# Kernel optimization log

Measured on AMD Instinct MI355X. Metric: run time of the kernel, lower is better.

The kernel has to match this reference:

```python
import jax, jax.numpy as jnp
import numpy as np

EMB = 1024
HEADS = 16
HEAD_DIM = EMB // HEADS
EPS = 1e-5


def setup_inputs() -> dict:
    key = jax.random.key(0)
    ks = jax.random.split(key, 10)
    B, T, D = 2, 2048, EMB
    s = 1.0 / np.sqrt(D)
    inp = {
        "x": jax.random.normal(ks[0], (B, T, D), dtype=jnp.float32),
        "wq": jax.random.normal(ks[1], (D, D), dtype=jnp.float32) * s,
        "bq": jnp.zeros((D,), jnp.float32),
        "wk": jax.random.normal(ks[2], (D, D), dtype=jnp.float32) * s,
        "bk": jnp.zeros((D,), jnp.float32),
        "wv": jax.random.normal(ks[3], (D, D), dtype=jnp.float32) * s,
        "bv": jnp.zeros((D,), jnp.float32),
        "wo": jax.random.normal(ks[4], (D, D), dtype=jnp.float32) * s,
        "bo": jnp.zeros((D,), jnp.float32),
        "gamma": jnp.ones((D,), jnp.float32),
        "beta": jnp.zeros((D,), jnp.float32),
    }
    return inp


def _attention(x, wq, bq, wk, bk, wv, bv, wo, bo, gamma, beta):
    B, T, D = x.shape
    H, Hd = HEADS, HEAD_DIM
    q = (x @ wq + bq).reshape(B, T, H, Hd)
    k = (x @ wk + bk).reshape(B, T, H, Hd)
    v = (x @ wv + bv).reshape(B, T, H, Hd)
    # scores: [B, H, T, T]
    scores = jnp.einsum("bthd,bshd->bhts", q, k) / np.sqrt(Hd)
    attn = jax.nn.softmax(scores, axis=-1)  # dropout is identity in eval
    ctx = jnp.einsum("bhts,bshd->bthd", attn, v).reshape(B, T, D)
    out = ctx @ wo + bo
    y = x + out  # residual (dropout identity)
    mu = jnp.mean(y, axis=-1, keepdims=True)
    var = jnp.var(y, axis=-1, keepdims=True)
    return (y - mu) * jax.lax.rsqrt(var + EPS) * gamma + beta


def reference(x, wq, bq, wk, bk, wv, bv, wo, bo, gamma, beta):
    return _attention(x, wq, bq, wk, bk, wv, bv, wo, bo, gamma, beta)
```

## Files before the change

### kernel.cpp

```cpp
#include <hip/hip_runtime.h>

#define BSZ   2
#define TSEQ  2048
#define DMOD  1024
#define NHEAD 16
#define HDIM  64
#define MROW  (BSZ*TSEQ)
#define LNEPS 1e-5f
#define QSCALE 0.18033688011f

typedef __bf16 bf16x8 __attribute__((ext_vector_type(8)));
typedef float  f32x4  __attribute__((ext_vector_type(4)));
typedef unsigned short us8 __attribute__((ext_vector_type(8)));
typedef unsigned short us4 __attribute__((ext_vector_type(4)));

__device__ __forceinline__ unsigned short f2bf(float f) {
    unsigned u = __float_as_uint(f);
    u += 0x7FFF + ((u >> 16) & 1);
    return (unsigned short)(u >> 16);
}
__device__ __forceinline__ float bf2f(unsigned short u) {
    return __uint_as_float((unsigned)u << 16);
}

__device__ __forceinline__ float fexp2(float x) {
#if __has_builtin(__builtin_amdgcn_exp2f)
    return __builtin_amdgcn_exp2f(x);
#else
    return __expf(x * 0.6931471805599453f);
#endif
}

__device__ __forceinline__ void gld_lds16(const void* g, void* l) {
    __builtin_amdgcn_global_load_lds(
        (const __attribute__((address_space(1))) unsigned int*)g,
        (__attribute__((address_space(3))) unsigned int*)l, 16, 0, 0);
}

__global__ __launch_bounds__(256) void prep_k(
    const float* __restrict__ x,
    const float* __restrict__ wq, const float* __restrict__ wk,
    const float* __restrict__ wv, const float* __restrict__ wo,
    unsigned short* __restrict__ Xb,
    unsigned short* __restrict__ WqkvT, unsigned short* __restrict__ WoT)
{
    const int tid = threadIdx.x;
    if (blockIdx.x < 2048) {
        const size_t i = ((size_t)blockIdx.x * 256 + tid) * 8;
        float4 a = *(const float4*)&x[i];
        float4 b = *(const float4*)&x[i + 4];
        union { unsigned short u[8]; uint4 v; } o;
        o.u[0]=f2bf(a.x); o.u[1]=f2bf(a.y); o.u[2]=f2bf(a.z); o.u[3]=f2bf(a.w);
        o.u[4]=f2bf(b.x); o.u[5]=f2bf(b.y); o.u[6]=f2bf(b.z); o.u[7]=f2bf(b.w);
        *(uint4*)&Xb[i] = o.v;
        return;
    }
    __shared__ float T[64][68];
    const int id = blockIdx.x - 2048;
    const int z  = id >> 8;
    const int bx = id & 15;
    const int by = (id >> 4) & 15;
    const float* W = (z == 0) ? wq : (z == 1) ? wk : (z == 2) ? wv : wo;
    unsigned short* Wt = (z < 3) ? (WqkvT + (size_t)z*1024*1024) : WoT;
    const int lr = tid >> 4, lc = (tid & 15) * 4;
    #pragma unroll
    for (int p = 0; p < 4; ++p) {
        const int kk = p*16 + lr;
        float4 v = *(const float4*)&W[(size_t)(by*64 + kk)*1024 + bx*64 + lc];
        T[lc+0][kk] = v.x; T[lc+1][kk] = v.y; T[lc+2][kk] = v.z; T[lc+3][kk] = v.w;
    }
    __syncthreads();
    #pragma unroll
    for (int p = 0; p < 2; ++p) {
        const int nl = p*32 + (tid >> 3);
        const int kb = (tid & 7) * 8;
        float4 a = *(const float4*)&T[nl][kb];
        float4 b = *(const float4*)&T[nl][kb+4];
        union { unsigned short u[8]; uint4 v; } o;
        o.u[0]=f2bf(a.x); o.u[1]=f2bf(a.y); o.u[2]=f2bf(a.z); o.u[3]=f2bf(a.w);
        o.u[4]=f2bf(b.x); o.u[5]=f2bf(b.y); o.u[6]=f2bf(b.z); o.u[7]=f2bf(b.w);
        *(uint4*)&Wt[(size_t)(bx*64 + nl)*1024 + by*64 + kb] = o.v;
    }
}


#define PH_SYNC() do { __builtin_amdgcn_s_barrier(); \
    asm volatile("s_waitcnt lgkmcnt(0)" ::: "memory"); \
    __builtin_amdgcn_sched_barrier(0); } while (0)

struct Core8 {
    const unsigned short *sA, *sB;
    unsigned short *A0w, *A1w, *B0w, *B1w;
    const unsigned short *fA0, *fA1, *fB0, *fB1;
    int swz0, swz1;
};

__device__ __forceinline__ void stage2(const unsigned short* s, unsigned short* d) {
    gld_lds16(s, d);
    gld_lds16(s + 64*1024, d + 4096);
}

__device__ __forceinline__ void core_setup(Core8& C, unsigned short* LDS,
    const unsigned short* A, const unsigned short* Bt, int bm, int bn, int kbase)
{
    const int tid = threadIdx.x;
    const int w = tid >> 6, lane = tid & 63;
    const int quad = lane >> 4, l16 = lane & 15;
    const int wm = w >> 2, wn = w & 3;
    const int r_l = lane >> 3, c_l = lane & 7;
    C.sA = A  + (size_t)(bm + w*8 + r_l)*1024 + (c_l ^ r_l)*8 + kbase;
    C.sB = Bt + (size_t)(bn + w*8 + r_l)*1024 + (c_l ^ r_l)*8 + kbase;
    unsigned short* A0 = LDS;
    unsigned short* A1 = LDS + 16384;
    unsigned short* B0 = LDS + 32768;
    unsigned short* B1 = LDS + 49152;
    C.A0w = A0 + w*512; C.A1w = A1 + w*512;
    C.B0w = B0 + w*512; C.B1w = B1 + w*512;
    C.fA0 = A0 + (wm*128 + l16)*64; C.fA1 = A1 + (wm*128 + l16)*64;
    C.fB0 = B0 + (wn*64 + l16)*64;  C.fB1 = B1 + (wn*64 + l16)*64;
    C.swz0 = ( quad      ^ (l16 & 7)) * 8;
    C.swz1 = ((4 + quad) ^ (l16 & 7)) * 8;
}

__device__ __forceinline__ void ld_b(const Core8& C, bf16x8 (&bfr)[4][2],
                                     const unsigned short* fB) {
    #pragma unroll
    for (int n = 0; n < 4; ++n) {
        bfr[n][0] = *(const bf16x8*)(fB + n*1024 + C.swz0);
        bfr[n][1] = *(const bf16x8*)(fB + n*1024 + C.swz1);
    }
}

template<int Q>
__device__ __forceinline__ void ld_a(const Core8& C, bf16x8 (&af)[2][2],
                                     const unsigned short* fA) {
    #pragma unroll
    for (int dm = 0; dm < 2; ++dm) {
        af[dm][0] = *(const bf16x8*)(fA + (Q*2+dm)*1024 + C.swz0);
        af[dm][1] = *(const bf16x8*)(fA + (Q*2+dm)*1024 + C.swz1);
    }
}

template<int Q>
__device__ __forceinline__ void mma_q(f32x4 (&acc)[8][4], bf16x8 (&af)[2][2],
                                      bf16x8 (&bfr)[4][2]) {
    __builtin_amdgcn_s_setprio(1);
    #pragma unroll
    for (int dm = 0; dm < 2; ++dm)
        #pragma unroll
        for (int n = 0; n < 4; ++n) {
            f32x4 t = acc[Q*2+dm][n];
            t = __builtin_amdgcn_mfma_f32_16x16x32_bf16(af[dm][0], bfr[n][0], t, 0, 0, 0);
            t = __builtin_amdgcn_mfma_f32_16x16x32_bf16(af[dm][1], bfr[n][1], t, 0, 0, 0);
            acc[Q*2+dm][n] = t;
        }
    __builtin_amdgcn_s_setprio(0);
}

template<int NIT>
__device__ __forceinline__ void core_kloop(const Core8& C, f32x4 (&acc)[8][4])
{
    stage2(C.sA,                 C.A0w);
    stage2(C.sA + 128*1024,      C.A0w + 8192);
    stage2(C.sB,                 C.B0w);
    stage2(C.sB + 128*1024,      C.B0w + 8192);
    stage2(C.sB + 64,            C.B1w);
    stage2(C.sB + 128*1024 + 64, C.B1w + 8192);
    asm volatile("s_waitcnt vmcnt(4)" ::: "memory");
    __builtin_amdgcn_s_barrier();

    bf16x8 bfr[4][2];
    bf16x8 af[2][2];

    #pragma unroll 1
    for (int it = 0; it < NIT - 1; ++it) {
        const int kk = it * 128;
        ld_b(C, bfr, C.fB0);
        ld_a<0>(C, af, C.fA0);
        stage2(C.sA + kk + 64,            C.A1w);
        stage2(C.sA + 128*1024 + kk + 64, C.A1w + 8192);
        PH_SYNC();  mma_q<0>(acc, af, bfr);
        __builtin_amdgcn_s_barrier();
        ld_a<1>(C, af, C.fA0);
        stage2(C.sB + kk + 128, C.B0w);
        PH_SYNC();  mma_q<1>(acc, af, bfr);
        __builtin_amdgcn_s_barrier();
        ld_a<2>(C, af, C.fA0);
        stage2(C.sB + 128*1024 + kk + 128, C.B0w + 8192);
        PH_SYNC();  mma_q<2>(acc, af, bfr);
        __builtin_amdgcn_s_barrier();
        ld_a<3>(C, af, C.fA0);
        PH_SYNC();  mma_q<3>(acc, af, bfr);
        asm volatile("s_waitcnt vmcnt(4)" ::: "memory");
        __builtin_amdgcn_s_barrier();
        ld_b(C, bfr, C.fB1);
        ld_a<0>(C, af, C.fA1);
        stage2(C.sA + kk + 128,            C.A0w);
        stage2(C.sA + 128*1024 + kk + 128, C.A0w + 8192);
        PH_SYNC();  mma_q<0>(acc, af, bfr);
        __builtin_amdgcn_s_barrier();
        ld_a<1>(C, af, C.fA1);
        stage2(C.sB + kk + 192, C.B1w);
        PH_SYNC();  mma_q<1>(acc, af, bfr);
        __builtin_amdgcn_s_barrier();
        ld_a<2>(C, af, C.fA1);
        stage2(C.sB + 128*1024 + kk + 192, C.B1w + 8192);
        PH_SYNC();  mma_q<2>(acc, af, bfr);
        __builtin_amdgcn_s_barrier();
        ld_a<3>(C, af, C.fA1);
        PH_SYNC();  mma_q<3>(acc, af, bfr);
        asm volatile("s_waitcnt vmcnt(4)" ::: "memory");
        __builtin_amdgcn_s_barrier();
    }

    {
        const int kk = (NIT - 1) * 128;
        ld_b(C, bfr, C.fB0);
        ld_a<0>(C, af, C.fA0);
        stage2(C.sA + kk + 64,            C.A1w);
        stage2(C.sA + 128*1024 + kk + 64, C.A1w + 8192);
        PH_SYNC();  mma_q<0>(acc, af, bfr);
        __builtin_amdgcn_s_barrier();
        ld_a<1>(C, af, C.fA0); PH_SYNC(); mma_q<1>(acc, af, bfr); __builtin_amdgcn_s_barrier();
        ld_a<2>(C, af, C.fA0); PH_SYNC(); mma_q<2>(acc, af, bfr); __builtin_amdgcn_s_barrier();
        ld_a<3>(C, af, C.fA0); PH_SYNC(); mma_q<3>(acc, af, bfr);
        asm volatile("s_waitcnt vmcnt(0)" ::: "memory");
        __builtin_amdgcn_s_barrier();
        ld_b(C, bfr, C.fB1);
        ld_a<0>(C, af, C.fA1); PH_SYNC(); mma_q<0>(acc, af, bfr); __builtin_amdgcn_s_barrier();
        ld_a<1>(C, af, C.fA1); PH_SYNC(); mma_q<1>(acc, af, bfr); __builtin_amdgcn_s_barrier();
        ld_a<2>(C, af, C.fA1); PH_SYNC(); mma_q<2>(acc, af, bfr); __builtin_amdgcn_s_barrier();
        ld_a<3>(C, af, C.fA1); PH_SYNC(); mma_q<3>(acc, af, bfr);
    }
}

__global__ __launch_bounds__(512, 2) void gemm_qkv_k(
    const unsigned short* __restrict__ A, const unsigned short* __restrict__ Bt,
    const float* __restrict__ b0, const float* __restrict__ b1,
    const float* __restrict__ b2,
    unsigned short* __restrict__ oQ, unsigned short* __restrict__ oK,
    unsigned short* __restrict__ oV)
{
    extern __shared__ unsigned short LDS[];
    const int ob = blockIdx.x;
    const int wg = (ob & 7) * 24 + (ob >> 3);
    const int by = wg / 12, bx = wg - by*12;
    const int bm = by * 256, bn = bx * 256;

    Core8 C;
    core_setup(C, LDS, A, Bt, bm, bn, 0);

    f32x4 acc[8][4];
    #pragma unroll
    for (int i = 0; i < 8; ++i)
        #pragma unroll
        for (int j = 0; j < 4; ++j) acc[i][j] = (f32x4){0.f,0.f,0.f,0.f};

    core_kloop<8>(C, acc);

    const int tid = threadIdx.x;
    const int w = tid >> 6, lane = tid & 63;
    const int quad = lane >> 4, l16 = lane & 15;
    const int wm = w >> 2, wn = w & 3;
    const int seg = bn >> 10;
    const int cb  = bn & 1023;
    if (seg < 2) {
        unsigned short* O = (seg == 0) ? oQ : oK;
        const float sc = (seg == 0) ? QSCALE : 1.0f;
        const float* bias = (seg == 0) ? b0 : b1;
        #pragma unroll
        for (int n = 0; n < 4; ++n) {
            const int col = cb + wn*64 + n*16 + l16;
            const float bs = bias[col];
            #pragma unroll
            for (int m = 0; m < 8; ++m)
                #pragma unroll
                for (int r = 0; r < 4; ++r) {
                    const int grow = bm + wm*128 + m*16 + quad*4 + r;
                    O[(size_t)grow*1024 + col] = f2bf((acc[m][n][r] + bs) * sc);
                }
        }
    } else {
        #pragma unroll
        for (int n = 0; n < 4; ++n) {
            const int ch = cb + wn*64 + n*16 + l16;
            const float bs = b2[ch];
            #pragma unroll
            for (int m = 0; m < 8; ++m) {
                const int grow0 = bm + wm*128 + m*16 + quad*4;
                us4 o;
                #pragma unroll
                for (int r = 0; r < 4; ++r) o[r] = f2bf(acc[m][n][r] + bs);
                *(us4*)&oV[(size_t)ch*MROW + grow0] = o;
            }
        }
    }
}

__global__ __launch_bounds__(512, 2) void gemm_proj_k(
    const unsigned short* __restrict__ A, const unsigned short* __restrict__ Bt,
    unsigned short* __restrict__ P)
{
    extern __shared__ unsigned short LDS[];
    const int ob = blockIdx.x;
    const int wg = (ob & 7) * 8 + (ob >> 3);
    const int by = wg >> 2, bx = wg & 3;
    const int kz = blockIdx.y;
    const int bm = by * 256, bn = bx * 256;

    Core8 C;
    core_setup(C, LDS, A, Bt, bm, bn, kz * 256);

    f32x4 acc[8][4];
    #pragma unroll
    for (int i = 0; i < 8; ++i)
        #pragma unroll
        for (int j = 0; j < 4; ++j) acc[i][j] = (f32x4){0.f,0.f,0.f,0.f};

    core_kloop<2>(C, acc);

    const int tid = threadIdx.x;
    const int w = tid >> 6, lane = tid & 63;
    const int quad = lane >> 4, l16 = lane & 15;
    const int wm = w >> 2, wn = w & 3;
    unsigned short* O = P + (size_t)kz*MROW*1024;
    #pragma unroll
    for (int n = 0; n < 4; ++n) {
        const int col = bn + wn*64 + n*16 + l16;
        #pragma unroll
        for (int m = 0; m < 8; ++m)
            #pragma unroll
            for (int r = 0; r < 4; ++r) {
                const int grow = bm + wm*128 + m*16 + quad*4 + r;
                O[(size_t)grow*1024 + col] = f2bf(acc[m][n][r]);
            }
    }
}

__global__ __launch_bounds__(256, 2) void attn_k(
    const unsigned short* __restrict__ Qg,
    const unsigned short* __restrict__ Kg,
    const unsigned short* __restrict__ Vtg,
    unsigned short* __restrict__ CTX)
{
    extern __shared__ __align__(16) char lds_raw[];
    unsigned short* KV = (unsigned short*)lds_raw;
    unsigned short* Qs = (unsigned short*)lds_raw;
    float* Od = (float*)lds_raw;
    float* Ld = (float*)(lds_raw + 65536);

    const int tid  = threadIdx.x;
    const int wv   = tid >> 6;
    const int lane = tid & 63;
    const int quad = lane >> 4;
    const int l16  = lane & 15;
    const int wq   = wv & 1;
    const int wk   = wv >> 1;
    const int qb   = blockIdx.x * 128;
    const int h    = blockIdx.y;
    const int b    = blockIdx.z;

    {
        const int row = tid & 127, cb = (tid >> 7) * 32;
        const unsigned short* Qrow = Qg + ((size_t)(b*TSEQ + qb + row))*DMOD + h*HDIM + cb;
        #pragma unroll
        for (int j = 0; j < 4; ++j)
            *(us8*)&Qs[row*72 + cb + j*8] = *(const us8*)&Qrow[j*8];
    }
    __syncthreads();
    bf16x8 qf[4][2];
    #pragma unroll
    for (int nt = 0; nt < 4; ++nt)
        #pragma unroll
        for (int kh = 0; kh < 2; ++kh)
            qf[nt][kh] = *(const bf16x8*)&Qs[(wq*64 + nt*16 + l16)*72 + kh*32 + quad*8];
    __syncthreads();

    const int sr = lane >> 3;
    const int sc = lane & 7;
    const bool isK = (wv < 2);
    const int half = wv & 1;
    const unsigned short* gbase;
    unsigned int goff[8];
    unsigned short* ldstb;
    if (isK) {
        gbase = Kg + ((size_t)(b*TSEQ + half*1024))*DMOD + h*HDIM;
        #pragma unroll
        for (int s = 0; s < 8; ++s) {
            const int R = s*8 + sr;
            const int gc = sc ^ ((R ^ (R >> 2)) & 7);
            goff[s] = (unsigned)(R*DMOD + gc*8);
        }
        ldstb = KV + half*4096;
    } else {
        gbase = Vtg + ((size_t)(h*HDIM))*MROW + b*TSEQ + half*1024;
        #pragma unroll
        for (int s = 0; s < 8; ++s) {
            const int D = s*8 + sr;
            const int gc = sc ^ (D & 7);
            goff[s] = (unsigned)(D*MROW + gc*8);
        }
        ldstb = KV + 16384 + half*4096;
    }
    const size_t gstep = isK ? (size_t)64*DMOD : (size_t)64;

    const int rowA_l = (l16 >> 2)*8 + (l16 & 3);
    const int rowB_l = rowA_l + 4;
    const int swA = (rowA_l ^ (rowA_l >> 2)) & 7;
    const int swB = (rowB_l ^ (rowB_l >> 2)) & 7;

    bf16x8 onef;
    { union { unsigned short u[8]; bf16x8 v; } o1;
      #pragma unroll
      for (int i = 0; i < 8; ++i) o1.u[i] = 0x3F80;
      onef = o1.v; }

    f32x4 oacc[4][4];
    f32x4 lacc[4];
    #pragma unroll
    for (int dt = 0; dt < 4; ++dt)
        #pragma unroll
        for (int nt = 0; nt < 4; ++nt) oacc[dt][nt] = (f32x4){0.f,0.f,0.f,0.f};
    #pragma unroll
    for (int nt = 0; nt < 4; ++nt) lacc[nt] = (f32x4){0.f,0.f,0.f,0.f};

    #pragma unroll
    for (int s = 0; s < 8; ++s)
        gld_lds16(gbase + goff[s], ldstb + s*512);
    __syncthreads();

    for (int it = 0; it < 16; ++it) {
        const int cbuf = (it & 1) * 8192;
        if (it < 15) {
            const unsigned short* gn = gbase + (size_t)(it+1)*gstep;
            unsigned short* d = ldstb + (cbuf ^ 8192);
            #pragma unroll
            for (int s = 0; s < 8; ++s)
                gld_lds16(gn + goff[s], d + s*512);
        }
        __builtin_amdgcn_sched_barrier(0);
        const unsigned short* KsW = KV + cbuf + wk*4096;
        const unsigned short* VsW = KV + 16384 + cbuf + wk*4096;

        #pragma unroll
        for (int gl = 0; gl < 2; ++gl) {
            const int rA = gl*32 + rowA_l;
            const int rB = gl*32 + rowB_l;
            bf16x8 ka0 = *(const bf16x8*)&KsW[rA*64 + ((quad     ^ swA))*8];
            bf16x8 ka1 = *(const bf16x8*)&KsW[rA*64 + (((4+quad) ^ swA))*8];
            bf16x8 kb0 = *(const bf16x8*)&KsW[rB*64 + ((quad     ^ swB))*8];
            bf16x8 kb1 = *(const bf16x8*)&KsW[rB*64 + (((4+quad) ^ swB))*8];
            bf16x8 vf[4];
            #pragma unroll
            for (int dt = 0; dt < 4; ++dt)
                vf[dt] = *(const bf16x8*)&VsW[(dt*16 + l16)*64 + ((gl*4 + quad) ^ (l16 & 7))*8];

            #pragma unroll
            for (int nt = 0; nt < 4; ++nt) {
                __builtin_amdgcn_s_setprio(1);
                f32x4 z = (f32x4){0.f,0.f,0.f,0.f};
                z = __builtin_amdgcn_mfma_f32_16x16x32_bf16(ka0, qf[nt][0], z, 0, 0, 0);
                f32x4 sA = __builtin_amdgcn_mfma_f32_16x16x32_bf16(ka1, qf[nt][1], z, 0, 0, 0);
                z = (f32x4){0.f,0.f,0.f,0.f};
                z = __builtin_amdgcn_mfma_f32_16x16x32_bf16(kb0, qf[nt][0], z, 0, 0, 0);
                f32x4 sB = __builtin_amdgcn_mfma_f32_16x16x32_bf16(kb1, qf[nt][1], z, 0, 0, 0);
                __builtin_amdgcn_s_setprio(0);

                float eA[4], eB[4];
                #pragma unroll
                for (int r = 0; r < 4; ++r) { eA[r] = fexp2(sA[r]); eB[r] = fexp2(sB[r]); }
                union { unsigned d[4]; bf16x8 v; } up;
                up.d[0] = __builtin_amdgcn_perm(__float_as_uint(eA[1]), __float_as_uint(eA[0]), 0x07060302);
                up.d[1] = __builtin_amdgcn_perm(__float_as_uint(eA[3]), __float_as_uint(eA[2]), 0x07060302);
                up.d[2] = __builtin_amdgcn_perm(__float_as_uint(eB[1]), __float_as_uint(eB[0]), 0x07060302);
                up.d[3] = __builtin_amdgcn_perm(__float_as_uint(eB[3]), __float_as_uint(eB[2]), 0x07060302);
                const bf16x8 pf = up.v;

                __builtin_amdgcn_s_setprio(1);
                lacc[nt] = __builtin_amdgcn_mfma_f32_16x16x32_bf16(onef, pf, lacc[nt], 0, 0, 0);
                #pragma unroll
                for (int dt = 0; dt < 4; ++dt)
                    oacc[dt][nt] = __builtin_amdgcn_mfma_f32_16x16x32_bf16(vf[dt], pf, oacc[dt][nt], 0, 0, 0);
                __builtin_amdgcn_s_setprio(0);
            }
        }
        __syncthreads();
    }

    if (wk == 0) {
        float* od = Od + wq*64*68;
        #pragma unroll
        for (int nt = 0; nt < 4; ++nt) {
            #pragma unroll
            for (int dt = 0; dt < 4; ++dt)
                *(f32x4*)&od[(nt*16 + l16)*68 + dt*16 + quad*4] = oacc[dt][nt];
            if (quad == 0) Ld[wq*64 + nt*16 + l16] = lacc[nt][0];
        }
    }
    __syncthreads();
    if (wk == 1) {
        const float* od = Od + wq*64*68;
        #pragma unroll
        for (int nt = 0; nt < 4; ++nt) {
            const float l = Ld[wq*64 + nt*16 + l16] + lacc[nt][0];
            const float inv = 1.f / l;
            const int q = qb + wq*64 + nt*16 + l16;
            unsigned short* crow = CTX + ((size_t)(b*TSEQ + q))*DMOD + h*HDIM;
            #pragma unroll
            for (int dt = 0; dt < 4; ++dt) {
                f32x4 p = *(const f32x4*)&od[(nt*16 + l16)*68 + dt*16 + quad*4];
                us4 o;
                #pragma unroll
                for (int r = 0; r < 4; ++r) o[r] = f2bf((p[r] + oacc[dt][nt][r]) * inv);
                *(us4*)&crow[dt*16 + quad*4] = o;
            }
        }
    }
}

__global__ __launch_bounds__(256) void red_ln_k(
    const float* __restrict__ x, const unsigned short* __restrict__ P,
    const float* __restrict__ bo,
    const float* __restrict__ gamma, const float* __restrict__ beta,
    float* __restrict__ out)
{
    __shared__ float rs[4], rss[4];
    const int row = blockIdx.x;
    const int tid = threadIdx.x;
    const int c = tid * 4;
    const float4 xv = *(const float4*)&x[(size_t)row*DMOD + c];
    const us4 p0 = *(const us4*)&P[(size_t)row*DMOD + c];
    const us4 p1 = *(const us4*)&P[(size_t)(MROW + row)*DMOD + c];
    const us4 p2 = *(const us4*)&P[(size_t)(2*MROW + row)*DMOD + c];
    const us4 p3 = *(const us4*)&P[(size_t)(3*MROW + row)*DMOD + c];
    const float4 bv4 = *(const float4*)&bo[c];
    const float v0 = xv.x + bf2f(p0[0]) + bf2f(p1[0]) + bf2f(p2[0]) + bf2f(p3[0]) + bv4.x;
    const float v1 = xv.y + bf2f(p0[1]) + bf2f(p1[1]) + bf2f(p2[1]) + bf2f(p3[1]) + bv4.y;
    const float v2 = xv.z + bf2f(p0[2]) + bf2f(p1[2]) + bf2f(p2[2]) + bf2f(p3[2]) + bv4.z;
    const float v3 = xv.w + bf2f(p0[3]) + bf2f(p1[3]) + bf2f(p2[3]) + bf2f(p3[3]) + bv4.w;
    float s  = v0 + v1 + v2 + v3;
    float ss = v0*v0 + v1*v1 + v2*v2 + v3*v3;
    #pragma unroll
    for (int o = 32; o > 0; o >>= 1) {
        s  += __shfl_down(s,  o, 64);
        ss += __shfl_down(ss, o, 64);
    }
    if ((tid & 63) == 0) { rs[tid >> 6] = s; rss[tid >> 6] = ss; }
    __syncthreads();
    s  = rs[0] + rs[1] + rs[2] + rs[3];
    ss = rss[0] + rss[1] + rss[2] + rss[3];
    const float mean = s * (1.f/DMOD);
    const float var  = ss * (1.f/DMOD) - mean*mean;
    const float rstd = rsqrtf(var + LNEPS);
    const float4 gv = *(const float4*)&gamma[c];
    const float4 bv = *(const float4*)&beta[c];
    float4 o;
    o.x = (v0 - mean)*rstd*gv.x + bv.x;
    o.y = (v1 - mean)*rstd*gv.y + bv.y;
    o.z = (v2 - mean)*rstd*gv.z + bv.z;
    o.w = (v3 - mean)*rstd*gv.w + bv.w;
    *(float4*)&out[(size_t)row*DMOD + c] = o;
}

extern "C" void kernel_launch(void* const* d_in, const int* in_sizes, int n_in,
                              void* d_out, int out_size, void* d_ws, size_t ws_size,
                              hipStream_t stream) {
    const float* x     = (const float*)d_in[0];
    const float* wq    = (const float*)d_in[1];
    const float* bq    = (const float*)d_in[2];
    const float* wk    = (const float*)d_in[3];
    const float* bk    = (const float*)d_in[4];
    const float* wvp   = (const float*)d_in[5];
    const float* bvp   = (const float*)d_in[6];
    const float* wo    = (const float*)d_in[7];
    const float* bo    = (const float*)d_in[8];
    const float* gamma = (const float*)d_in[9];
    const float* beta  = (const float*)d_in[10];
    float* out = (float*)d_out;

    unsigned short* Xb    = (unsigned short*)d_ws;
    unsigned short* WqkvT = Xb    + (size_t)MROW*DMOD;
    unsigned short* WoT   = WqkvT + (size_t)3072*1024;
    unsigned short* Qb    = WoT   + (size_t)1024*1024;
    unsigned short* Kb    = Qb    + (size_t)MROW*DMOD;
    unsigned short* VtG   = Kb    + (size_t)MROW*DMOD;
    unsigned short* CTXb  = VtG   + (size_t)DMOD*MROW;
    unsigned short* Pp    = CTXb  + (size_t)MROW*DMOD;

    prep_k<<<3072, 256, 0, stream>>>(x, wq, wk, wvp, wo, Xb, WqkvT, WoT);

    gemm_qkv_k<<<dim3(192), 512, 131072, stream>>>(
        Xb, WqkvT, bq, bk, bvp, Qb, Kb, VtG);

    attn_k<<<dim3(TSEQ/128, NHEAD, BSZ), 256, 66048, stream>>>(Qb, Kb, VtG, CTXb);

    gemm_proj_k<<<dim3(64, 4), 512, 131072, stream>>>(CTXb, WoT, Pp);

    red_ln_k<<<MROW, 256, 0, stream>>>(x, Pp, bo, gamma, beta, out);
}
```

Measured before the change: 191.9 us.

## Retile QKV GEMM to 256x192 tiles and batch attention exp/MFMA phases

The core GEMM loop is templated on the number of B sub-tiles, so the QKV projection now uses 256x192 output tiles. That gives 256 workgroups instead of 192, to fill the CUs more evenly, with smaller LDS and a launch bound of 1. The epilogue now picks the Q/K/V segment per 16-column fragment, since tiles can straddle segment boundaries. The attention inner loop is also restructured to issue all score MFMAs first, then all exp/pack work, then all PV MFMAs, exposing more independent work at the cost of extra registers.

```diff
diff --git a/kernel.cpp b/kernel.cpp
--- a/kernel.cpp
+++ b/kernel.cpp
@@ -88,19 +88,41 @@
     asm volatile("s_waitcnt lgkmcnt(0)" ::: "memory"); \
     __builtin_amdgcn_sched_barrier(0); } while (0)
 
-struct Core8 {
+template<int N>
+__device__ __forceinline__ void vmwait() {
+    if constexpr (N == 0)      asm volatile("s_waitcnt vmcnt(0)" ::: "memory");
+    else if constexpr (N == 3) asm volatile("s_waitcnt vmcnt(3)" ::: "memory");
+    else                       asm volatile("s_waitcnt vmcnt(4)" ::: "memory");
+}
+
+template<int NB>
+struct CoreT {
     const unsigned short *sA, *sB;
     unsigned short *A0w, *A1w, *B0w, *B1w;
     const unsigned short *fA0, *fA1, *fB0, *fB1;
     int swz0, swz1;
 };
 
-__device__ __forceinline__ void stage2(const unsigned short* s, unsigned short* d) {
-    gld_lds16(s, d);
-    gld_lds16(s + 64*1024, d + 4096);
-}
-
-__device__ __forceinline__ void core_setup(Core8& C, unsigned short* LDS,
+__device__ __forceinline__ void stageA4(const unsigned short* s, unsigned short* d) {
+    #pragma unroll
+    for (int u = 0; u < 4; ++u) gld_lds16(s + u*64*1024, d + u*4096);
+}
+template<int NB>
+__device__ __forceinline__ void stageBall(const unsigned short* s, unsigned short* d) {
+    #pragma unroll
+    for (int u = 0; u < NB; ++u) gld_lds16(s + u*64*1024, d + u*4096);
+}
+__device__ __forceinline__ void stageB01(const unsigned short* s, unsigned short* d) {
+    gld_lds16(s, d); gld_lds16(s + 64*1024, d + 4096);
+}
+template<int NB>
+__device__ __forceinline__ void stageBrest(const unsigned short* s, unsigned short* d) {
+    #pragma unroll
+    for (int u = 2; u < NB; ++u) gld_lds16(s + u*64*1024, d + u*4096);
+}
+
+template<int NB>
+__device__ __forceinline__ void core_setup(CoreT<NB>& C, unsigned short* LDS,
     const unsigned short* A, const unsigned short* Bt, int bm, int bn, int kbase)
 {
     const int tid = threadIdx.x;
@@ -113,26 +135,27 @@
     unsigned short* A0 = LDS;
     unsigned short* A1 = LDS + 16384;
     unsigned short* B0 = LDS + 32768;
-    unsigned short* B1 = LDS + 49152;
+    unsigned short* B1 = B0 + NB*4096;
     C.A0w = A0 + w*512; C.A1w = A1 + w*512;
     C.B0w = B0 + w*512; C.B1w = B1 + w*512;
     C.fA0 = A0 + (wm*128 + l16)*64; C.fA1 = A1 + (wm*128 + l16)*64;
-    C.fB0 = B0 + (wn*64 + l16)*64;  C.fB1 = B1 + (wn*64 + l16)*64;
+    C.fB0 = B0 + (wn*NB*16 + l16)*64;  C.fB1 = B1 + (wn*NB*16 + l16)*64;
     C.swz0 = ( quad      ^ (l16 & 7)) * 8;
     C.swz1 = ((4 + quad) ^ (l16 & 7)) * 8;
 }
 
-__device__ __forceinline__ void ld_b(const Core8& C, bf16x8 (&bfr)[4][2],
+template<int NB>
+__device__ __forceinline__ void ld_b(const CoreT<NB>& C, bf16x8 (&bfr)[NB][2],
                                      const unsigned short* fB) {
     #pragma unroll
-    for (int n = 0; n < 4; ++n) {
+    for (int n = 0; n < NB; ++n) {
         bfr[n][0] = *(const bf16x8*)(fB + n*1024 + C.swz0);
         bfr[n][1] = *(const bf16x8*)(fB + n*1024 + C.swz1);
     }
 }
 
-template<int Q>
-__device__ __forceinline__ void ld_a(const Core8& C, bf16x8 (&af)[2][2],
+template<int Q, int NB>
+__device__ __forceinline__ void ld_a(const CoreT<NB>& C, bf16x8 (&af)[2][2],
                                      const unsigned short* fA) {
     #pragma unroll
     for (int dm = 0; dm < 2; ++dm) {
@@ -141,14 +164,14 @@
     }
 }
 
-template<int Q>
-__device__ __forceinline__ void mma_q(f32x4 (&acc)[8][4], bf16x8 (&af)[2][2],
-                                      bf16x8 (&bfr)[4][2]) {
+template<int Q, int NB>
+__device__ __forceinline__ void mma_q(f32x4 (&acc)[8][NB], bf16x8 (&af)[2][2],
+                                      bf16x8 (&bfr)[NB][2]) {
     __builtin_amdgcn_s_setprio(1);
     #pragma unroll
     for (int dm = 0; dm < 2; ++dm)
         #pragma unroll
-        for (int n = 0; n < 4; ++n) {
+        for (int n = 0; n < NB; ++n) {
             f32x4 t = acc[Q*2+dm][n];
             t = __builtin_amdgcn_mfma_f32_16x16x32_bf16(af[dm][0], bfr[n][0], t, 0, 0, 0);
             t = __builtin_amdgcn_mfma_f32_16x16x32_bf16(af[dm][1], bfr[n][1], t, 0, 0, 0);
@@ -157,84 +180,78 @@
     __builtin_amdgcn_s_setprio(0);
 }
 
-template<int NIT>
-__device__ __forceinline__ void core_kloop(const Core8& C, f32x4 (&acc)[8][4])
+template<int NIT, int NB>
+__device__ __forceinline__ void core_kloop(const CoreT<NB>& C, f32x4 (&acc)[8][NB])
 {
-    stage2(C.sA,                 C.A0w);
-    stage2(C.sA + 128*1024,      C.A0w + 8192);
-    stage2(C.sB,                 C.B0w);
-    stage2(C.sB + 128*1024,      C.B0w + 8192);
-    stage2(C.sB + 64,            C.B1w);
-    stage2(C.sB + 128*1024 + 64, C.B1w + 8192);
-    asm volatile("s_waitcnt vmcnt(4)" ::: "memory");
+    stageA4(C.sA, C.A0w);
+    stageBall<NB>(C.sB,      C.B0w);
+    stageBall<NB>(C.sB + 64, C.B1w);
+    vmwait<NB>();
     __builtin_amdgcn_s_barrier();
 
-    bf16x8 bfr[4][2];
+    bf16x8 bfr[NB][2];
     bf16x8 af[2][2];
 
     #pragma unroll 1
     for (int it = 0; it < NIT - 1; ++it) {
         const int kk = it * 128;
-        ld_b(C, bfr, C.fB0);
-        ld_a<0>(C, af, C.fA0);
-        stage2(C.sA + kk + 64,            C.A1w);
-        stage2(C.sA + 128*1024 + kk + 64, C.A1w + 8192);
-        PH_SYNC();  mma_q<0>(acc, af, bfr);
-        __builtin_amdgcn_s_barrier();
-        ld_a<1>(C, af, C.fA0);
-        stage2(C.sB + kk + 128, C.B0w);
-        PH_SYNC();  mma_q<1>(acc, af, bfr);
-        __builtin_amdgcn_s_barrier();
-        ld_a<2>(C, af, C.fA0);
-        stage2(C.sB + 128*1024 + kk + 128, C.B0w + 8192);
-        PH_SYNC();  mma_q<2>(acc, af, bfr);
-        __builtin_amdgcn_s_barrier();
-        ld_a<3>(C, af, C.fA0);
-        PH_SYNC();  mma_q<3>(acc, af, bfr);
-        asm volatile("s_waitcnt vmcnt(4)" ::: "memory");
-        __builtin_amdgcn_s_barrier();
-        ld_b(C, bfr, C.fB1);
-        ld_a<0>(C, af, C.fA1);
-        stage2(C.sA + kk + 128,            C.A0w);
-        stage2(C.sA + 128*1024 + kk + 128, C.A0w + 8192);
-        PH_SYNC();  mma_q<0>(acc, af, bfr);
-        __builtin_amdgcn_s_barrier();
-        ld_a<1>(C, af, C.fA1);
-        stage2(C.sB + kk + 192, C.B1w);
-        PH_SYNC();  mma_q<1>(acc, af, bfr);
-        __builtin_amdgcn_s_barrier();
-        ld_a<2>(C, af, C.fA1);
-        stage2(C.sB + 128*1024 + kk + 192, C.B1w + 8192);
-        PH_SYNC();  mma_q<2>(acc, af, bfr);
-        __builtin_amdgcn_s_barrier();
-        ld_a<3>(C, af, C.fA1);
-        PH_SYNC();  mma_q<3>(acc, af, bfr);
-        asm volatile("s_waitcnt vmcnt(4)" ::: "memory");
+        ld_b<NB>(C, bfr, C.fB0);
+        ld_a<0,NB>(C, af, C.fA0);
+        stageA4(C.sA + kk + 64, C.A1w);
+        PH_SYNC();  mma_q<0,NB>(acc, af, bfr);
+        __builtin_amdgcn_s_barrier();
+        ld_a<1,NB>(C, af, C.fA0);
+        stageB01(C.sB + kk + 128, C.B0w);
+        PH_SYNC();  mma_q<1,NB>(acc, af, bfr);
+        __builtin_amdgcn_s_barrier();
+        ld_a<2,NB>(C, af, C.fA0);
+        stageBrest<NB>(C.sB + kk + 128, C.B0w);
+        PH_SYNC();  mma_q<2,NB>(acc, af, bfr);
+        __builtin_amdgcn_s_barrier();
+        ld_a<3,NB>(C, af, C.fA0);
+        PH_SYNC();  mma_q<3,NB>(acc, af, bfr);
+        vmwait<NB>();
+        __builtin_amdgcn_s_barrier();
+        ld_b<NB>(C, bfr, C.fB1);
+        ld_a<0,NB>(C, af, C.fA1);
+        stageA4(C.sA + kk + 128, C.A0w);
+        PH_SYNC();  mma_q<0,NB>(acc, af, bfr);
+        __builtin_amdgcn_s_barrier();
+        ld_a<1,NB>(C, af, C.fA1);
+        stageB01(C.sB + kk + 192, C.B1w);
+        PH_SYNC();  mma_q<1,NB>(acc, af, bfr);
+        __builtin_amdgcn_s_barrier();
+        ld_a<2,NB>(C, af, C.fA1);
+        stageBrest<NB>(C.sB + kk + 192, C.B1w);
+        PH_SYNC();  mma_q<2,NB>(acc, af, bfr);
+        __builtin_amdgcn_s_barrier();
+        ld_a<3,NB>(C, af, C.fA1);
+        PH_SYNC();  mma_q<3,NB>(acc, af, bfr);
+        vmwait<NB>();
         __builtin_amdgcn_s_barrier();
     }
 
     {
         const int kk = (NIT - 1) * 128;
-        ld_b(C, bfr, C.fB0);
-        ld_a<0>(C, af, C.fA0);
-        stage2(C.sA + kk + 64,            C.A1w);
-        stage2(C.sA + 128*1024 + kk + 64, C.A1w + 8192);
-        PH_SYNC();  mma_q<0>(acc, af, bfr);
-        __builtin_amdgcn_s_barrier();
-        ld_a<1>(C, af, C.fA0); PH_SYNC(); mma_q<1>(acc, af, bfr); __builtin_amdgcn_s_barrier();
-        ld_a<2>(C, af, C.fA0); PH_SYNC(); mma_q<2>(acc, af, bfr); __builtin_amdgcn_s_barrier();
-        ld_a<3>(C, af, C.fA0); PH_SYNC(); mma_q<3>(acc, af, bfr);
-        asm volatile("s_waitcnt vmcnt(0)" ::: "memory");
-        __builtin_amdgcn_s_barrier();
-        ld_b(C, bfr, C.fB1);
-        ld_a<0>(C, af, C.fA1); PH_SYNC(); mma_q<0>(acc, af, bfr); __builtin_amdgcn_s_barrier();
-        ld_a<1>(C, af, C.fA1); PH_SYNC(); mma_q<1>(acc, af, bfr); __builtin_amdgcn_s_barrier();
-        ld_a<2>(C, af, C.fA1); PH_SYNC(); mma_q<2>(acc, af, bfr); __builtin_amdgcn_s_barrier();
-        ld_a<3>(C, af, C.fA1); PH_SYNC(); mma_q<3>(acc, af, bfr);
-    }
-}
-
-__global__ __launch_bounds__(512, 2) void gemm_qkv_k(
+        ld_b<NB>(C, bfr, C.fB0);
+        ld_a<0,NB>(C, af, C.fA0);
+        stageA4(C.sA + kk + 64, C.A1w);
+        PH_SYNC();  mma_q<0,NB>(acc, af, bfr);
+        __builtin_amdgcn_s_barrier();
+        ld_a<1,NB>(C, af, C.fA0); PH_SYNC(); mma_q<1,NB>(acc, af, bfr); __builtin_amdgcn_s_barrier();
+        ld_a<2,NB>(C, af, C.fA0); PH_SYNC(); mma_q<2,NB>(acc, af, bfr); __builtin_amdgcn_s_barrier();
+        ld_a<3,NB>(C, af, C.fA0); PH_SYNC(); mma_q<3,NB>(acc, af, bfr);
+        vmwait<0>();
+        __builtin_amdgcn_s_barrier();
+        ld_b<NB>(C, bfr, C.fB1);
+        ld_a<0,NB>(C, af, C.fA1); PH_SYNC(); mma_q<0,NB>(acc, af, bfr); __builtin_amdgcn_s_barrier();
+        ld_a<1,NB>(C, af, C.fA1); PH_SYNC(); mma_q<1,NB>(acc, af, bfr); __builtin_amdgcn_s_barrier();
+        ld_a<2,NB>(C, af, C.fA1); PH_SYNC(); mma_q<2,NB>(acc, af, bfr); __builtin_amdgcn_s_barrier();
+        ld_a<3,NB>(C, af, C.fA1); PH_SYNC(); mma_q<3,NB>(acc, af, bfr);
+    }
+}
+
+__global__ __launch_bounds__(512, 1) void gemm_qkv_k(
     const unsigned short* __restrict__ A, const unsigned short* __restrict__ Bt,
     const float* __restrict__ b0, const float* __restrict__ b1,
     const float* __restrict__ b2,
@@ -243,34 +260,35 @@
 {
     extern __shared__ unsigned short LDS[];
     const int ob = blockIdx.x;
-    const int wg = (ob & 7) * 24 + (ob >> 3);
-    const int by = wg / 12, bx = wg - by*12;
-    const int bm = by * 256, bn = bx * 256;
-
-    Core8 C;
-    core_setup(C, LDS, A, Bt, bm, bn, 0);
-
-    f32x4 acc[8][4];
+    const int wg = (ob & 7) * 32 + (ob >> 3);
+    const int by = wg >> 4, bx = wg & 15;
+    const int bm = by * 256, bn = bx * 192;
+
+    CoreT<3> C;
+    core_setup<3>(C, LDS, A, Bt, bm, bn, 0);
+
+    f32x4 acc[8][3];
     #pragma unroll
     for (int i = 0; i < 8; ++i)
         #pragma unroll
-        for (int j = 0; j < 4; ++j) acc[i][j] = (f32x4){0.f,0.f,0.f,0.f};
-
-    core_kloop<8>(C, acc);
+        for (int j = 0; j < 3; ++j) acc[i][j] = (f32x4){0.f,0.f,0.f,0.f};
+
+    core_kloop<8,3>(C, acc);
 
     const int tid = threadIdx.x;
     const int w = tid >> 6, lane = tid & 63;
     const int quad = lane >> 4, l16 = lane & 15;
     const int wm = w >> 2, wn = w & 3;
-    const int seg = bn >> 10;
-    const int cb  = bn & 1023;
-    if (seg < 2) {
-        unsigned short* O = (seg == 0) ? oQ : oK;
-        const float sc = (seg == 0) ? QSCALE : 1.0f;
-        const float* bias = (seg == 0) ? b0 : b1;
-        #pragma unroll
-        for (int n = 0; n < 4; ++n) {
-            const int col = cb + wn*64 + n*16 + l16;
+    #pragma unroll
+    for (int n = 0; n < 3; ++n) {
+        const int c0  = bn + wn*48 + n*16;
+        const int seg = c0 >> 10;
+        const int cl0 = c0 & 1023;
+        if (seg < 2) {
+            unsigned short* O = (seg == 0) ? oQ : oK;
+            const float sc = (seg == 0) ? QSCALE : 1.0f;
+            const float* bias = (seg == 0) ? b0 : b1;
+            const int col = cl0 + l16;
             const float bs = bias[col];
             #pragma unroll
             for (int m = 0; m < 8; ++m)
@@ -279,11 +297,8 @@
                     const int grow = bm + wm*128 + m*16 + quad*4 + r;
                     O[(size_t)grow*1024 + col] = f2bf((acc[m][n][r] + bs) * sc);
                 }
-        }
-    } else {
-        #pragma unroll
-        for (int n = 0; n < 4; ++n) {
-            const int ch = cb + wn*64 + n*16 + l16;
+        } else {
+            const int ch = cl0 + l16;
             const float bs = b2[ch];
             #pragma unroll
             for (int m = 0; m < 8; ++m) {
@@ -308,8 +323,8 @@
     const int kz = blockIdx.y;
     const int bm = by * 256, bn = bx * 256;
 
-    Core8 C;
-    core_setup(C, LDS, A, Bt, bm, bn, kz * 256);
+    CoreT<4> C;
+    core_setup<4>(C, LDS, A, Bt, bm, bn, kz * 256);
 
     f32x4 acc[8][4];
     #pragma unroll
@@ -317,7 +332,7 @@
         #pragma unroll
         for (int j = 0; j < 4; ++j) acc[i][j] = (f32x4){0.f,0.f,0.f,0.f};
 
-    core_kloop<2>(C, acc);
+    core_kloop<2,4>(C, acc);
 
     const int tid = threadIdx.x;
     const int w = tid >> 6, lane = tid & 63;
@@ -455,34 +470,38 @@
             for (int dt = 0; dt < 4; ++dt)
                 vf[dt] = *(const bf16x8*)&VsW[(dt*16 + l16)*64 + ((gl*4 + quad) ^ (l16 & 7))*8];
 
+            f32x4 sA[4], sB[4];
             #pragma unroll
             for (int nt = 0; nt < 4; ++nt) {
-                __builtin_amdgcn_s_setprio(1);
                 f32x4 z = (f32x4){0.f,0.f,0.f,0.f};
                 z = __builtin_amdgcn_mfma_f32_16x16x32_bf16(ka0, qf[nt][0], z, 0, 0, 0);
-                f32x4 sA = __builtin_amdgcn_mfma_f32_16x16x32_bf16(ka1, qf[nt][1], z, 0, 0, 0);
-                z = (f32x4){0.f,0.f,0.f,0.f};
-                z = __builtin_amdgcn_mfma_f32_16x16x32_bf16(kb0, qf[nt][0], z, 0, 0, 0);
-                f32x4 sB = __builtin_amdgcn_mfma_f32_16x16x32_bf16(kb1, qf[nt][1], z, 0, 0, 0);
-                __builtin_amdgcn_s_setprio(0);
-
+                sA[nt] = __builtin_amdgcn_mfma_f32_16x16x32_bf16(ka1, qf[nt][1], z, 0, 0, 0);
+                f32x4 z2 = (f32x4){0.f,0.f,0.f,0.f};
+                z2 = __builtin_amdgcn_mfma_f32_16x16x32_bf16(kb0, qf[nt][0], z2, 0, 0, 0);
+                sB[nt] = __builtin_amdgcn_mfma_f32_16x16x32_bf16(kb1, qf[nt][1], z2, 0, 0, 0);
+            }
+            bf16x8 pf[4];
+            #pragma unroll
+            for (int nt = 0; nt < 4; ++nt) {
                 float eA[4], eB[4];
                 #pragma unroll
-                for (int r = 0; r < 4; ++r) { eA[r] = fexp2(sA[r]); eB[r] = fexp2(sB[r]); }
+                for (int r = 0; r < 4; ++r) { eA[r] = fexp2(sA[nt][r]); eB[r] = fexp2(sB[nt][r]); }
                 union { unsigned d[4]; bf16x8 v; } up;
                 up.d[0] = __builtin_amdgcn_perm(__float_as_uint(eA[1]), __float_as_uint(eA[0]), 0x07060302);
                 up.d[1] = __builtin_amdgcn_perm(__float_as_uint(eA[3]), __float_as_uint(eA[2]), 0x07060302);
                 up.d[2] = __builtin_amdgcn_perm(__float_as_uint(eB[1]), __float_as_uint(eB[0]), 0x07060302);
                 up.d[3] = __builtin_amdgcn_perm(__float_as_uint(eB[3]), __float_as_uint(eB[2]), 0x07060302);
-                const bf16x8 pf = up.v;
-
-                __builtin_amdgcn_s_setprio(1);
-                lacc[nt] = __builtin_amdgcn_mfma_f32_16x16x32_bf16(onef, pf, lacc[nt], 0, 0, 0);
+                pf[nt] = up.v;
+            }
+            __builtin_amdgcn_s_setprio(1);
+            #pragma unroll
+            for (int nt = 0; nt < 4; ++nt) {
+                lacc[nt] = __builtin_amdgcn_mfma_f32_16x16x32_bf16(onef, pf[nt], lacc[nt], 0, 0, 0);
                 #pragma unroll
                 for (int dt = 0; dt < 4; ++dt)
-                    oacc[dt][nt] = __builtin_amdgcn_mfma_f32_16x16x32_bf16(vf[dt], pf, oacc[dt][nt], 0, 0, 0);
-                __builtin_amdgcn_s_setprio(0);
+                    oacc[dt][nt] = __builtin_amdgcn_mfma_f32_16x16x32_bf16(vf[dt], pf[nt], oacc[dt][nt], 0, 0, 0);
             }
+            __builtin_amdgcn_s_setprio(0);
         }
         __syncthreads();
     }
@@ -589,7 +608,7 @@
 
     prep_k<<<3072, 256, 0, stream>>>(x, wq, wk, wvp, wo, Xb, WqkvT, WoT);
 
-    gemm_qkv_k<<<dim3(192), 512, 131072, stream>>>(
+    gemm_qkv_k<<<dim3(256), 512, 114688, stream>>>(
         Xb, WqkvT, bq, bk, bvp, Qb, Kb, VtG);
 
     attn_k<<<dim3(TSEQ/128, NHEAD, BSZ), 256, 66048, stream>>>(Qb, Kb, VtG, CTXb);
```

Measured after the change: 193.7 us. About the same (+0.9%).
